# Performance work log

Measured on AMD Instinct MI355X. Metric: run time of the kernel, lower is better.

Reference implementation:

```python
import jax, jax.numpy as jnp
import numpy as np

T, B = 256, 128
VOCAB, E, H, L = 73640, 320, 512, 5
G = 4 * H  # gate dim 2048


def setup_inputs() -> dict:
    key = jax.random.key(0)
    ks = jax.random.split(key, 12)
    stdv = 1.0 / np.sqrt(H)
    u = lambda k, shape: jax.random.uniform(k, shape, jnp.float32, -stdv, stdv)
    tokens = jax.random.randint(ks[0], (T, B), 0, VOCAB)
    embed = jax.random.normal(ks[1], (VOCAB, E), jnp.float32) * 0.1
    # layer 0 (input dim E), directions stacked on axis 0
    W_ih0 = u(ks[2], (2, G, E))
    W_hh0 = u(ks[3], (2, G, H))
    b_ih0 = u(ks[4], (2, G))
    b_hh0 = u(ks[5], (2, G))
    # layers 1..4 (input dim 2H = concat of both directions)
    W_ih = u(ks[6], (L - 1, 2, G, 2 * H))
    W_hh = u(ks[7], (L - 1, 2, G, H))
    b_ih = u(ks[8], (L - 1, 2, G))
    b_hh = u(ks[9], (L - 1, 2, G))
    return {"tokens": tokens, "embed": embed, "W_ih0": W_ih0, "W_hh0": W_hh0,
            "b_ih0": b_ih0, "b_hh0": b_hh0, "W_ih": W_ih, "W_hh": W_hh,
            "b_ih": b_ih, "b_hh": b_hh}


def _lstm_both_dirs(x, h, c, Wi, Wh, bi, bh):
    # x: [B, in]; h, c: [2, B, H]; Wi: [2, 4H, in]; Wh: [2, 4H, H]; bi, bh: [2, 4H]
    gates = (jnp.einsum('bi,dgi->dbg', x, Wi)
             + jnp.einsum('dbh,dgh->dbg', h, Wh)
             + (bi + bh)[:, None, :])
    i, f, g, o = jnp.split(gates, 4, axis=-1)  # PyTorch gate order i,f,g,o
    c_new = jax.nn.sigmoid(f) * c + jax.nn.sigmoid(i) * jnp.tanh(g)
    h_new = jax.nn.sigmoid(o) * jnp.tanh(c_new)
    return h_new, c_new


def reference(tokens, embed, W_ih0, W_hh0, b_ih0, b_hh0, W_ih, W_hh, b_ih, b_hh):
    emb = embed[tokens]  # [T, B, E]
    Bsz = tokens.shape[1]
    h0 = jnp.zeros((L, 2, Bsz, H), jnp.float32)
    c0 = jnp.zeros((L, 2, Bsz, H), jnp.float32)

    def step(carry, x_t):
        h, c = carry
        hl, cl = _lstm_both_dirs(x_t, h[0], c[0], W_ih0, W_hh0, b_ih0, b_hh0)
        hs, cs = [hl], [cl]
        inp = jnp.concatenate([hl[0], hl[1]], axis=-1)  # [B, 2H]
        for l in range(L - 1):
            hl, cl = _lstm_both_dirs(inp, h[l + 1], c[l + 1],
                                     W_ih[l], W_hh[l], b_ih[l], b_hh[l])
            hs.append(hl); cs.append(cl)
            inp = jnp.concatenate([hl[0], hl[1]], axis=-1)
        return (jnp.stack(hs), jnp.stack(cs)), hs[-1]  # emit last-layer h [2, B, H]

    _, last_layer_h = jax.lax.scan(step, (h0, c0), emb)  # [T, 2, B, H]
    # LASEREmbedderI: take last layer, max-pool over the two directions
    return jnp.max(last_layer_h, axis=1)  # [T, B, H]
```

## Files before the change

### kernel.cpp

```cpp
#include <hip/hip_runtime.h>
#include <stdint.h>

typedef unsigned short u16;
typedef unsigned int   u32;
typedef unsigned long long u64;
typedef short bf16x8 __attribute__((ext_vector_type(8)));
typedef float f32x4  __attribute__((ext_vector_type(4)));

static_assert(sizeof(bf16x8) == 16, "bf16x8 must be 16B");

#define LOG2E 1.4426950408889634f
#define TCH 32
#define NSLOT 131072
#define HDIR  65536

__device__ __forceinline__ float bf2f(u16 u) { return __builtin_bit_cast(float, ((u32)u) << 16); }
__device__ __forceinline__ u16 f2bf(float f) {
  u32 x = __builtin_bit_cast(u32, f);
  return (u16)((x + 0x7fffu + ((x >> 16) & 1u)) >> 16);
}
__device__ __forceinline__ float sigm(float x) {
  return __builtin_amdgcn_rcpf(1.f + __builtin_amdgcn_exp2f(-LOG2E * x));
}
__device__ __forceinline__ float tanh_(float x) {
  return 1.f - 2.f * __builtin_amdgcn_rcpf(1.f + __builtin_amdgcn_exp2f(2.f * LOG2E * x));
}
__device__ __forceinline__ bf16x8 cvt8(const float* p) {
  bf16x8 r;
  #pragma unroll
  for (int j = 0; j < 8; ++j) r[j] = (short)f2bf(p[j]);
  return r;
}

__global__ void k_bias(const float* __restrict__ bi0, const float* __restrict__ bh0,
                       const float* __restrict__ bi, const float* __restrict__ bh,
                       float* __restrict__ out) {
  int i = blockIdx.x * blockDim.x + threadIdx.x;
  if (i < 4096) out[i] = bi0[i] + bh0[i];
  else if (i < 20480) out[i] = bi[i - 4096] + bh[i - 4096];
}

__device__ __forceinline__ void gemm_tile(
    u16* smem, const u16* hb, const float* emb, const int* tok,
    const float* Wif, const float* bias, u16* gx, int K, int t0,
    int d, int nt0, int tt)
{
  u16* As = smem;
  u16* Bs = smem + 8192;
  int* s_tok = (int*)(smem + 16384);
  int tid = threadIdx.x, lane = tid & 63, w = tid >> 6;
  int wm = w & 1, wn = w >> 1;
  int t = t0 + tt;
  if (tok && tid < 128) s_tok[tid] = tok[t * 128 + tid];
  __syncthreads();

  const float* Bbase = Wif + ((size_t)d * 2048 + nt0 * 128) * K;
  f32x4 acc[4][4];
  #pragma unroll
  for (int a = 0; a < 4; ++a)
    #pragma unroll
    for (int b = 0; b < 4; ++b) acc[a][b] = f32x4{0.f, 0.f, 0.f, 0.f};

  int nkt = K >> 6;
  for (int kt = 0; kt < nkt; ++kt) {
    #pragma unroll
    for (int i = 0; i < 4; ++i) {
      int s = tid + i * 256;
      int row = s >> 3, c = s & 7;
      int cs = c ^ (row & 7);
      bf16x8 va;
      if (tok) {
        va = cvt8(emb + (size_t)s_tok[row] * 320 + kt * 64 + c * 8);
      } else {
        int k = kt * 64 + c * 8;
        va = *(const bf16x8*)(hb + (size_t)(t + 1) * NSLOT + (size_t)(k >> 9) * HDIR
                              + (size_t)row * 512 + (k & 511));
      }
      bf16x8 vb = cvt8(Bbase + (size_t)row * K + kt * 64 + c * 8);
      *(bf16x8*)(&As[(row * 8 + cs) * 8]) = va;
      *(bf16x8*)(&Bs[(row * 8 + cs) * 8]) = vb;
    }
    __syncthreads();
    #pragma unroll
    for (int kk2 = 0; kk2 < 2; ++kk2) {
      int cl = kk2 * 4 + (lane >> 4);
      bf16x8 af[4], bfr[4];
      #pragma unroll
      for (int mt = 0; mt < 4; ++mt) {
        int row = wm * 64 + mt * 16 + (lane & 15);
        af[mt] = *(const bf16x8*)(&As[(row * 8 + (cl ^ (row & 7))) * 8]);
      }
      #pragma unroll
      for (int nt = 0; nt < 4; ++nt) {
        int row = wn * 64 + nt * 16 + (lane & 15);
        bfr[nt] = *(const bf16x8*)(&Bs[(row * 8 + (cl ^ (row & 7))) * 8]);
      }
      #pragma unroll
      for (int mt = 0; mt < 4; ++mt)
        #pragma unroll
        for (int nt = 0; nt < 4; ++nt)
          acc[mt][nt] = __builtin_amdgcn_mfma_f32_16x16x32_bf16(af[mt], bfr[nt], acc[mt][nt], 0, 0, 0);
    }
    __syncthreads();
  }
  #pragma unroll
  for (int nt = 0; nt < 4; ++nt) {
    int g = nt0 * 128 + wn * 64 + nt * 16 + (lane & 15);
    float bv = bias[d * 2048 + g];
    int q = g >> 9, hbb = (g >> 4) & 31, u = g & 15;
    size_t cb = (((size_t)d * 32 + hbb) * TCH + tt) * 8192;
    #pragma unroll
    for (int mt = 0; mt < 4; ++mt)
      #pragma unroll
      for (int r = 0; r < 4; ++r) {
        int b = wm * 64 + mt * 16 + (lane >> 4) * 4 + r;
        int ws2 = b >> 5, mts = (b >> 4) & 1, l4s = (b >> 2) & 3, rs = b & 3;
        gx[cb + (size_t)(ws2 * 64 + l4s * 16 + u) * 32 + mts * 16 + q * 4 + rs]
          = f2bf(acc[mt][nt][r] + bv);
      }
  }
}

__global__ __launch_bounds__(256) void k_gemm0(
    const float* __restrict__ emb, const int* __restrict__ tok,
    const float* __restrict__ Wif, const float* __restrict__ bias, u16* __restrict__ gx)
{
  __shared__ __align__(16) u16 smem[16640];
  int xt = blockIdx.x;
  gemm_tile(smem, nullptr, emb, tok, Wif, bias, gx, 320, 0, xt >> 4, xt & 15, blockIdx.y);
}

__device__ __forceinline__ void waitflags(const u32* fl, int lane, u32 target) {
  u32 v;
  do {
    v = (lane < 32)
      ? __hip_atomic_load(&fl[lane * 16], __ATOMIC_RELAXED, __HIP_MEMORY_SCOPE_AGENT)
      : target;
  } while (!__all((int)(v >= target)));
}

__global__ __launch_bounds__(256, 2) void k_fused(
    const float* __restrict__ Whf, const u16* __restrict__ gx_s,
    u16* __restrict__ hb, float* __restrict__ cbuf,
    u32* flags, u32 base, int t0, int hz,
    const float* __restrict__ emb, const int* __restrict__ tok_g,
    const float* __restrict__ Wif_g, const float* __restrict__ bias_g,
    u16* __restrict__ gx_g, int Kg, int t0g)
{
  __shared__ __align__(16) u16 smem[32768];
  int tid = threadIdx.x, lane = tid & 63, w = tid >> 6;

  if (blockIdx.x >= 64) {
    if (t0g < 0) return;
    #pragma unroll 1
    for (int i = 0; i < 4; ++i) {
      int tau = (blockIdx.x - 64) + i * 256;
      int xt = tau & 31, tt = tau >> 5;
      gemm_tile(smem, hb, emb, tok_g, Wif_g, bias_g, gx_g, Kg, t0g, xt >> 4, xt & 15, tt);
      __syncthreads();
    }
    return;
  }

  int d = blockIdx.x >> 5, hb_i = blockIdx.x & 31;
  const u32* fl = flags + d * 512;
  u32* myflag = flags + (d * 32 + hb_i) * 16;
  u16* WhL = smem;
  for (int i = tid; i < 64 * 512; i += 256) {
    int r = i >> 9, k = i & 511;
    int grow = (r >> 4) * 512 + hb_i * 16 + (r & 15);
    WhL[(r << 9) + (k ^ ((r & 7) << 3))] = f2bf(Whf[((size_t)d * 2048 + grow) * 512 + k]);
  }

  int bb = w * 32;
  int l15 = lane & 15, l4 = lane >> 4;
  float c2[2][4];
  if (t0 == 0) {
    #pragma unroll
    for (int mt = 0; mt < 2; ++mt)
      #pragma unroll
      for (int r = 0; r < 4; ++r) c2[mt][r] = 0.f;
  } else {
    #pragma unroll
    for (int mt = 0; mt < 2; ++mt)
      #pragma unroll
      for (int r = 0; r < 4; ++r) {
        int b = bb + mt * 16 + l4 * 4 + r;
        c2[mt][r] = cbuf[((size_t)d * 128 + b) * 512 + hb_i * 16 + l15];
      }
  }
  if (hz) {
    for (int i = tid; i < 512; i += 256) {
      int b = i >> 2, j = i & 3;
      u64* p = (u64*)(hb + (size_t)d * HDIR + (size_t)b * 512 + hb_i * 16) + j;
      __hip_atomic_store(p, 0ull, __ATOMIC_RELAXED, __HIP_MEMORY_SCOPE_AGENT);
    }
  }
  __syncthreads();
  if (hz && tid == 0)
    __hip_atomic_store(myflag, base + 1, __ATOMIC_RELAXED, __HIP_MEMORY_SCOPE_AGENT);
  int init1 = hz ? 1 : 0;

  const u16* gxblk = gx_s + ((size_t)d * 32 + hb_i) * TCH * 8192 + (size_t)tid * 32;
  bf16x8 gxv4[4], gxn4[4];
  #pragma unroll
  for (int j = 0; j < 4; ++j) gxv4[j] = *(const bf16x8*)(gxblk + j * 8);
  #pragma unroll
  for (int j = 0; j < 4; ++j) gxn4[j] = *(const bf16x8*)(gxblk + 8192 + j * 8);

  for (int tt = 0; tt < TCH; ++tt) {
    int t = t0 + tt;
    u32 target = base + (u32)tt + (u32)init1;
    if (!(tt == 0 && !init1)) waitflags(fl, lane, target);

    const u16* hp = hb + (size_t)t * NSLOT + (size_t)d * HDIR;
    const u16* hpA = hp + (size_t)(bb + l15) * 512 + l4 * 8;
    const u16* hpB = hp + (size_t)(bb + 16 + l15) * 512 + l4 * 8;
    f32x4 h0[16], h1[16];
    asm volatile(
      "global_load_dwordx4 %0, %8, off sc0 sc1\n\t"
      "global_load_dwordx4 %1, %8, off offset:64 sc0 sc1\n\t"
      "global_load_dwordx4 %2, %8, off offset:128 sc0 sc1\n\t"
      "global_load_dwordx4 %3, %8, off offset:192 sc0 sc1\n\t"
      "global_load_dwordx4 %4, %8, off offset:256 sc0 sc1\n\t"
      "global_load_dwordx4 %5, %8, off offset:320 sc0 sc1\n\t"
      "global_load_dwordx4 %6, %8, off offset:384 sc0 sc1\n\t"
      "global_load_dwordx4 %7, %8, off offset:448 sc0 sc1"
      : "=v"(h0[0]), "=v"(h0[1]), "=v"(h0[2]), "=v"(h0[3]),
        "=v"(h0[4]), "=v"(h0[5]), "=v"(h0[6]), "=v"(h0[7])
      : "v"(hpA) : "memory");
    asm volatile(
      "global_load_dwordx4 %0, %8, off offset:512 sc0 sc1\n\t"
      "global_load_dwordx4 %1, %8, off offset:576 sc0 sc1\n\t"
      "global_load_dwordx4 %2, %8, off offset:640 sc0 sc1\n\t"
      "global_load_dwordx4 %3, %8, off offset:704 sc0 sc1\n\t"
      "global_load_dwordx4 %4, %8, off offset:768 sc0 sc1\n\t"
      "global_load_dwordx4 %5, %8, off offset:832 sc0 sc1\n\t"
      "global_load_dwordx4 %6, %8, off offset:896 sc0 sc1\n\t"
      "global_load_dwordx4 %7, %8, off offset:960 sc0 sc1"
      : "=v"(h0[8]), "=v"(h0[9]), "=v"(h0[10]), "=v"(h0[11]),
        "=v"(h0[12]), "=v"(h0[13]), "=v"(h0[14]), "=v"(h0[15])
      : "v"(hpA) : "memory");
    asm volatile(
      "global_load_dwordx4 %0, %8, off sc0 sc1\n\t"
      "global_load_dwordx4 %1, %8, off offset:64 sc0 sc1\n\t"
      "global_load_dwordx4 %2, %8, off offset:128 sc0 sc1\n\t"
      "global_load_dwordx4 %3, %8, off offset:192 sc0 sc1\n\t"
      "global_load_dwordx4 %4, %8, off offset:256 sc0 sc1\n\t"
      "global_load_dwordx4 %5, %8, off offset:320 sc0 sc1\n\t"
      "global_load_dwordx4 %6, %8, off offset:384 sc0 sc1\n\t"
      "global_load_dwordx4 %7, %8, off offset:448 sc0 sc1"
      : "=v"(h1[0]), "=v"(h1[1]), "=v"(h1[2]), "=v"(h1[3]),
        "=v"(h1[4]), "=v"(h1[5]), "=v"(h1[6]), "=v"(h1[7])
      : "v"(hpB) : "memory");
    asm volatile(
      "global_load_dwordx4 %0, %8, off offset:512 sc0 sc1\n\t"
      "global_load_dwordx4 %1, %8, off offset:576 sc0 sc1\n\t"
      "global_load_dwordx4 %2, %8, off offset:640 sc0 sc1\n\t"
      "global_load_dwordx4 %3, %8, off offset:704 sc0 sc1\n\t"
      "global_load_dwordx4 %4, %8, off offset:768 sc0 sc1\n\t"
      "global_load_dwordx4 %5, %8, off offset:832 sc0 sc1\n\t"
      "global_load_dwordx4 %6, %8, off offset:896 sc0 sc1\n\t"
      "global_load_dwordx4 %7, %8, off offset:960 sc0 sc1\n\t"
      "s_waitcnt vmcnt(0)"
      : "=v"(h1[8]), "=v"(h1[9]), "=v"(h1[10]), "=v"(h1[11]),
        "=v"(h1[12]), "=v"(h1[13]), "=v"(h1[14]), "=v"(h1[15])
      : "v"(hpB) : "memory");
    __builtin_amdgcn_sched_barrier(0);

    f32x4 acc[2][4];
    #pragma unroll
    for (int mt = 0; mt < 2; ++mt)
      #pragma unroll
      for (int q = 0; q < 4; ++q) acc[mt][q] = f32x4{0.f, 0.f, 0.f, 0.f};
    #pragma unroll
    for (int kk = 0; kk < 16; ++kk) {
      int kbase = kk * 32 + l4 * 8;
      bf16x8 a0 = __builtin_bit_cast(bf16x8, h0[kk]);
      bf16x8 a1 = __builtin_bit_cast(bf16x8, h1[kk]);
      #pragma unroll
      for (int q = 0; q < 4; ++q) {
        int r = q * 16 + l15;
        bf16x8 bv = *(const bf16x8*)(&WhL[(r << 9) + (kbase ^ ((r & 7) << 3))]);
        acc[0][q] = __builtin_amdgcn_mfma_f32_16x16x32_bf16(a0, bv, acc[0][q], 0, 0, 0);
        acc[1][q] = __builtin_amdgcn_mfma_f32_16x16x32_bf16(a1, bv, acc[1][q], 0, 0, 0);
      }
    }
    u16* ho = hb + (size_t)(t + 1) * NSLOT + (size_t)d * HDIR;
    u32 hvv[2][4];
    #pragma unroll
    for (int mt = 0; mt < 2; ++mt)
      #pragma unroll
      for (int r = 0; r < 4; ++r) {
        float gi = acc[mt][0][r] + bf2f((u16)gxv4[mt * 2][r]);
        float gf = acc[mt][1][r] + bf2f((u16)gxv4[mt * 2][4 + r]);
        float gg = acc[mt][2][r] + bf2f((u16)gxv4[mt * 2 + 1][r]);
        float go = acc[mt][3][r] + bf2f((u16)gxv4[mt * 2 + 1][4 + r]);
        float cn = sigm(gf) * c2[mt][r] + sigm(gi) * tanh_(gg);
        float hn = sigm(go) * tanh_(cn);
        c2[mt][r] = cn;
        hvv[mt][r] = (u32)f2bf(hn);
      }
    {
      u16* st0 = ho + (size_t)(bb + l4 * 4) * 512 + hb_i * 16 + l15;
      u16* st1 = st0 + 16 * 512;
      int tt2 = (tt + 2 < TCH) ? (tt + 2) : (TCH - 1);
      const u16* gaddr = gxblk + (size_t)tt2 * 8192;
      f32x4 g0, g1, g2, g3;
      asm volatile(
        "global_store_short %12, %4, off sc0 sc1\n\t"
        "global_store_short %12, %5, off offset:1024 sc0 sc1\n\t"
        "global_store_short %12, %6, off offset:2048 sc0 sc1\n\t"
        "global_store_short %12, %7, off offset:3072 sc0 sc1\n\t"
        "global_store_short %13, %8, off sc0 sc1\n\t"
        "global_store_short %13, %9, off offset:1024 sc0 sc1\n\t"
        "global_store_short %13, %10, off offset:2048 sc0 sc1\n\t"
        "global_store_short %13, %11, off offset:3072 sc0 sc1\n\t"
        "global_load_dwordx4 %0, %14, off\n\t"
        "global_load_dwordx4 %1, %14, off offset:16\n\t"
        "global_load_dwordx4 %2, %14, off offset:32\n\t"
        "global_load_dwordx4 %3, %14, off offset:48\n\t"
        "s_waitcnt vmcnt(4)"
        : "=&v"(g0), "=&v"(g1), "=&v"(g2), "=&v"(g3)
        : "v"(hvv[0][0]), "v"(hvv[0][1]), "v"(hvv[0][2]), "v"(hvv[0][3]),
          "v"(hvv[1][0]), "v"(hvv[1][1]), "v"(hvv[1][2]), "v"(hvv[1][3]),
          "v"(st0), "v"(st1), "v"(gaddr)
        : "memory");
      __syncthreads();
      if (tid == 0)
        __hip_atomic_store(myflag, target + 1, __ATOMIC_RELAXED, __HIP_MEMORY_SCOPE_AGENT);
      #pragma unroll
      for (int j = 0; j < 4; ++j) gxv4[j] = gxn4[j];
      gxn4[0] = __builtin_bit_cast(bf16x8, g0);
      gxn4[1] = __builtin_bit_cast(bf16x8, g1);
      gxn4[2] = __builtin_bit_cast(bf16x8, g2);
      gxn4[3] = __builtin_bit_cast(bf16x8, g3);
    }
  }
  #pragma unroll
  for (int mt = 0; mt < 2; ++mt)
    #pragma unroll
    for (int r = 0; r < 4; ++r) {
      int b = bb + mt * 16 + l4 * 4 + r;
      cbuf[((size_t)d * 128 + b) * 512 + hb_i * 16 + l15] = c2[mt][r];
    }
}

__global__ void k_final(const u16* __restrict__ hb, float* __restrict__ out, int n) {
  int i = blockIdx.x * 256 + threadIdx.x;
  if (i >= n) return;
  int t = i >> 16, rem = i & 65535;
  int b = rem >> 9, j = rem & 511;
  const u16* s = hb + (size_t)(t + 1) * NSLOT + (size_t)b * 512 + j;
  float a = bf2f(s[0]);
  float bv = bf2f(s[HDIR]);
  out[i] = fmaxf(a, bv);
}

extern "C" void kernel_launch(void* const* d_in, const int* in_sizes, int n_in,
                              void* d_out, int out_size, void* d_ws, size_t ws_size,
                              hipStream_t stream) {
  (void)in_sizes; (void)n_in; (void)out_size; (void)ws_size;
  const int*   tokens = (const int*)d_in[0];
  const float* embedW = (const float*)d_in[1];
  const float* W_ih0  = (const float*)d_in[2];
  const float* W_hh0  = (const float*)d_in[3];
  const float* b_ih0  = (const float*)d_in[4];
  const float* b_hh0  = (const float*)d_in[5];
  const float* W_ih   = (const float*)d_in[6];
  const float* W_hh   = (const float*)d_in[7];
  const float* b_ih   = (const float*)d_in[8];
  const float* b_hh   = (const float*)d_in[9];

  char* ws = (char*)d_ws;
  size_t off = 0;
  auto alloc = [&](size_t bytes) { void* p = ws + off; off += (bytes + 255) & ~(size_t)255; return p; };
  float* biasC = (float*)alloc(20480ull * 4);
  u16*   hbuf  = (u16*)alloc((size_t)257 * NSLOT * 2);
  u16*   gxA   = (u16*)alloc(16777216ull * 2);
  u16*   gxB   = (u16*)alloc(16777216ull * 2);
  float* cbuf  = (float*)alloc(131072ull * 4);
  u32*   flags = (u32*)alloc(8192);

  hipMemsetAsync(flags, 0, 8192, stream);
  k_bias<<<80, 256, 0, stream>>>(b_ih0, b_hh0, b_ih, b_hh, biasC);
  k_gemm0<<<dim3(32, 32), 256, 0, stream>>>(embedW, tokens, W_ih0, biasC, gxA);

  u32 base = 0;
  for (int l = 0; l < 5; ++l) {
    const float* Whf_l = l ? (W_hh + (size_t)(l - 1) * 2097152) : W_hh0;
    for (int c = 0; c < 8; ++c) {
      int g = l * 8 + c;
      u16* gx_s = (g & 1) ? gxB : gxA;
      u16* gx_g = (g & 1) ? gxA : gxB;
      int lg = (c < 7) ? l : l + 1;
      int cg = (c < 7) ? c + 1 : 0;
      int has_g = (lg <= 4);
      const float* Wif_g = (lg == 0) ? W_ih0 : (W_ih + (size_t)(lg - 1) * 4194304);
      const int* tok_g = (lg == 0) ? tokens : nullptr;
      int Kg = (lg == 0) ? 320 : 1024;
      k_fused<<<320, 256, 0, stream>>>(
          Whf_l, gx_s, hbuf, cbuf, flags, base, c * TCH, (l == 0 && c == 0) ? 1 : 0,
          embedW, tok_g, Wif_g, biasC + (size_t)lg * 4096, gx_g, Kg,
          has_g ? cg * TCH : -1);
      base += 64;
    }
  }
  k_final<<<65536, 256, 0, stream>>>(hbuf, (float*)d_out, 16777216);
}
```

Measured before the change: 11.04 ms.

## Use per-wave flags to remove block barrier from recurrent step

Each wave now publishes its own progress flag, written from inside the store asm after its h stores. Consumers poll the matching wave's flag across all 32 producer blocks. This removes the per-step __syncthreads and the single-thread flag store, so waves in a block can proceed independently through the serial recurrence. It also adds s_sleep backoff in the polling loop and raises wave priority. The trade-off is reliance on store ordering within a wave for correctness, plus a changed base increment whose consistency with flag resets is delicate.

```diff
diff --git a/kernel.cpp b/kernel.cpp
--- a/kernel.cpp
+++ b/kernel.cpp
@@ -130,13 +130,15 @@
   gemm_tile(smem, nullptr, emb, tok, Wif, bias, gx, 320, 0, xt >> 4, xt & 15, blockIdx.y);
 }
 
-__device__ __forceinline__ void waitflags(const u32* fl, int lane, u32 target) {
+__device__ __forceinline__ void waitflags(const u32* fl, int lane, int w, u32 target) {
+  const u32* p = fl + ((lane & 31) << 4) + w;
   u32 v;
-  do {
-    v = (lane < 32)
-      ? __hip_atomic_load(&fl[lane * 16], __ATOMIC_RELAXED, __HIP_MEMORY_SCOPE_AGENT)
-      : target;
-  } while (!__all((int)(v >= target)));
+  for (;;) {
+    asm volatile("global_load_dword %0, %1, off sc0 sc1\n\ts_waitcnt vmcnt(0)"
+                 : "=v"(v) : "v"(p) : "memory");
+    if (__all((int)(v >= target))) break;
+    __builtin_amdgcn_s_sleep(1);
+  }
 }
 
 __global__ __launch_bounds__(256, 2) void k_fused(
@@ -164,7 +166,7 @@
 
   int d = blockIdx.x >> 5, hb_i = blockIdx.x & 31;
   const u32* fl = flags + d * 512;
-  u32* myflag = flags + (d * 32 + hb_i) * 16;
+  u32* myflag = flags + d * 512 + hb_i * 16 + w;
   u16* WhL = smem;
   for (int i = tid; i < 64 * 512; i += 256) {
     int r = i >> 9, k = i & 511;
@@ -197,9 +199,12 @@
     }
   }
   __syncthreads();
-  if (hz && tid == 0)
-    __hip_atomic_store(myflag, base + 1, __ATOMIC_RELAXED, __HIP_MEMORY_SCOPE_AGENT);
+  if (hz && lane == 0) {
+    u32 iv = base + 1;
+    asm volatile("global_store_dword %0, %1, off sc0 sc1" :: "v"(myflag), "v"(iv) : "memory");
+  }
   int init1 = hz ? 1 : 0;
+  __builtin_amdgcn_s_setprio(1);
 
   const u16* gxblk = gx_s + ((size_t)d * 32 + hb_i) * TCH * 8192 + (size_t)tid * 32;
   bf16x8 gxv4[4], gxn4[4];
@@ -211,7 +216,7 @@
   for (int tt = 0; tt < TCH; ++tt) {
     int t = t0 + tt;
     u32 target = base + (u32)tt + (u32)init1;
-    if (!(tt == 0 && !init1)) waitflags(fl, lane, target);
+    if (!(tt == 0 && !init1)) waitflags(fl, lane, w, target);
 
     const u16* hp = hb + (size_t)t * NSLOT + (size_t)d * HDIR;
     const u16* hpA = hp + (size_t)(bb + l15) * 512 + l4 * 8;
@@ -226,8 +231,8 @@
       "global_load_dwordx4 %5, %8, off offset:320 sc0 sc1\n\t"
       "global_load_dwordx4 %6, %8, off offset:384 sc0 sc1\n\t"
       "global_load_dwordx4 %7, %8, off offset:448 sc0 sc1"
-      : "=v"(h0[0]), "=v"(h0[1]), "=v"(h0[2]), "=v"(h0[3]),
-        "=v"(h0[4]), "=v"(h0[5]), "=v"(h0[6]), "=v"(h0[7])
+      : "=&v"(h0[0]), "=&v"(h0[1]), "=&v"(h0[2]), "=&v"(h0[3]),
+        "=&v"(h0[4]), "=&v"(h0[5]), "=&v"(h0[6]), "=&v"(h0[7])
       : "v"(hpA) : "memory");
     asm volatile(
       "global_load_dwordx4 %0, %8, off offset:512 sc0 sc1\n\t"
@@ -238,8 +243,8 @@
       "global_load_dwordx4 %5, %8, off offset:832 sc0 sc1\n\t"
       "global_load_dwordx4 %6, %8, off offset:896 sc0 sc1\n\t"
       "global_load_dwordx4 %7, %8, off offset:960 sc0 sc1"
-      : "=v"(h0[8]), "=v"(h0[9]), "=v"(h0[10]), "=v"(h0[11]),
-        "=v"(h0[12]), "=v"(h0[13]), "=v"(h0[14]), "=v"(h0[15])
+      : "=&v"(h0[8]), "=&v"(h0[9]), "=&v"(h0[10]), "=&v"(h0[11]),
+        "=&v"(h0[12]), "=&v"(h0[13]), "=&v"(h0[14]), "=&v"(h0[15])
       : "v"(hpA) : "memory");
     asm volatile(
       "global_load_dwordx4 %0, %8, off sc0 sc1\n\t"
@@ -250,8 +255,8 @@
       "global_load_dwordx4 %5, %8, off offset:320 sc0 sc1\n\t"
       "global_load_dwordx4 %6, %8, off offset:384 sc0 sc1\n\t"
       "global_load_dwordx4 %7, %8, off offset:448 sc0 sc1"
-      : "=v"(h1[0]), "=v"(h1[1]), "=v"(h1[2]), "=v"(h1[3]),
-        "=v"(h1[4]), "=v"(h1[5]), "=v"(h1[6]), "=v"(h1[7])
+      : "=&v"(h1[0]), "=&v"(h1[1]), "=&v"(h1[2]), "=&v"(h1[3]),
+        "=&v"(h1[4]), "=&v"(h1[5]), "=&v"(h1[6]), "=&v"(h1[7])
       : "v"(hpB) : "memory");
     asm volatile(
       "global_load_dwordx4 %0, %8, off offset:512 sc0 sc1\n\t"
@@ -263,8 +268,8 @@
       "global_load_dwordx4 %6, %8, off offset:896 sc0 sc1\n\t"
       "global_load_dwordx4 %7, %8, off offset:960 sc0 sc1\n\t"
       "s_waitcnt vmcnt(0)"
-      : "=v"(h1[8]), "=v"(h1[9]), "=v"(h1[10]), "=v"(h1[11]),
-        "=v"(h1[12]), "=v"(h1[13]), "=v"(h1[14]), "=v"(h1[15])
+      : "=&v"(h1[8]), "=&v"(h1[9]), "=&v"(h1[10]), "=&v"(h1[11]),
+        "=&v"(h1[12]), "=&v"(h1[13]), "=&v"(h1[14]), "=&v"(h1[15])
       : "v"(hpB) : "memory");
     __builtin_amdgcn_sched_barrier(0);
 
@@ -306,29 +311,28 @@
       u16* st1 = st0 + 16 * 512;
       int tt2 = (tt + 2 < TCH) ? (tt + 2) : (TCH - 1);
       const u16* gaddr = gxblk + (size_t)tt2 * 8192;
+      u32 fv = target + 1;
       f32x4 g0, g1, g2, g3;
       asm volatile(
-        "global_store_short %12, %4, off sc0 sc1\n\t"
-        "global_store_short %12, %5, off offset:1024 sc0 sc1\n\t"
-        "global_store_short %12, %6, off offset:2048 sc0 sc1\n\t"
-        "global_store_short %12, %7, off offset:3072 sc0 sc1\n\t"
-        "global_store_short %13, %8, off sc0 sc1\n\t"
-        "global_store_short %13, %9, off offset:1024 sc0 sc1\n\t"
-        "global_store_short %13, %10, off offset:2048 sc0 sc1\n\t"
-        "global_store_short %13, %11, off offset:3072 sc0 sc1\n\t"
-        "global_load_dwordx4 %0, %14, off\n\t"
-        "global_load_dwordx4 %1, %14, off offset:16\n\t"
-        "global_load_dwordx4 %2, %14, off offset:32\n\t"
-        "global_load_dwordx4 %3, %14, off offset:48\n\t"
-        "s_waitcnt vmcnt(4)"
+        "global_store_short %13, %4, off sc0 sc1\n\t"
+        "global_store_short %13, %5, off offset:1024 sc0 sc1\n\t"
+        "global_store_short %13, %6, off offset:2048 sc0 sc1\n\t"
+        "global_store_short %13, %7, off offset:3072 sc0 sc1\n\t"
+        "global_store_short %14, %8, off sc0 sc1\n\t"
+        "global_store_short %14, %9, off offset:1024 sc0 sc1\n\t"
+        "global_store_short %14, %10, off offset:2048 sc0 sc1\n\t"
+        "global_store_short %14, %11, off offset:3072 sc0 sc1\n\t"
+        "global_load_dwordx4 %0, %15, off\n\t"
+        "global_load_dwordx4 %1, %15, off offset:16\n\t"
+        "global_load_dwordx4 %2, %15, off offset:32\n\t"
+        "global_load_dwordx4 %3, %15, off offset:48\n\t"
+        "s_waitcnt vmcnt(4)\n\t"
+        "global_store_dword %16, %12, off sc0 sc1"
         : "=&v"(g0), "=&v"(g1), "=&v"(g2), "=&v"(g3)
         : "v"(hvv[0][0]), "v"(hvv[0][1]), "v"(hvv[0][2]), "v"(hvv[0][3]),
           "v"(hvv[1][0]), "v"(hvv[1][1]), "v"(hvv[1][2]), "v"(hvv[1][3]),
-          "v"(st0), "v"(st1), "v"(gaddr)
+          "v"(fv), "v"(st0), "v"(st1), "v"(gaddr), "v"(myflag)
         : "memory");
-      __syncthreads();
-      if (tid == 0)
-        __hip_atomic_store(myflag, target + 1, __ATOMIC_RELAXED, __HIP_MEMORY_SCOPE_AGENT);
       #pragma unroll
       for (int j = 0; j < 4; ++j) gxv4[j] = gxn4[j];
       gxn4[0] = __builtin_bit_cast(bf16x8, g0);
@@ -403,7 +407,7 @@
           Whf_l, gx_s, hbuf, cbuf, flags, base, c * TCH, (l == 0 && c == 0) ? 1 : 0,
           embedW, tok_g, Wif_g, biasC + (size_t)lg * 4096, gx_g, Kg,
           has_g ? cg * TCH : -1);
-      base += 64;
+      base += 40;
     }
   }
   k_final<<<65536, 256, 0, stream>>>(hbuf, (float*)d_out, 16777216);
```

Result: faster. 10.25 ms (-7.2%).
